# Performance work log

Hardware: AMD Instinct MI355X
Metric: run time of the kernel (lower is better)

Reference implementation:

```python
import jax, jax.numpy as jnp
import numpy as np

EMBED_DIM = 1024
FFN_DIM = 4096
N_QUBITS = 10


def setup_inputs() -> dict:
    key = jax.random.key(0)
    k_x, k_phi, k_w1, k_w2 = jax.random.split(key, 4)
    x = jax.random.normal(k_x, (8, 2048, EMBED_DIM), dtype=jnp.float32)
    # trainable RY angles, one per wire (torchquantum init ~ U(0, 2pi); any init works for a reference)
    ry_params = jax.random.uniform(k_phi, (N_QUBITS,), dtype=jnp.float32, minval=0.0, maxval=2.0 * np.pi)
    # nn.Linear(n_qubits, ffn_dim, bias=False): weight [ffn_dim, n_qubits]
    w1 = jax.random.normal(k_w1, (FFN_DIM, N_QUBITS), dtype=jnp.float32) / np.sqrt(N_QUBITS)
    # nn.Linear(ffn_dim, embed_dim, bias=False): weight [embed_dim, ffn_dim]
    w2 = jax.random.normal(k_w2, (EMBED_DIM, FFN_DIM), dtype=jnp.float32) / np.sqrt(FFN_DIM)
    return {"x": x, "ry_params": ry_params, "w1": w1, "w2": w2}


def reference(x, ry_params, w1, w2):
    # Quantum layer in closed form: wires are unentangled.
    # |0> --RX(x_i)--RY(phi_i)--> <Z_i> = cos(x_i) * cos(phi_i)
    # Only the first N_QUBITS features of each token are encoded.
    q_out = jnp.cos(x[..., :N_QUBITS]) * jnp.cos(ry_params)  # [B, S, nq]
    # dropout is identity in eval mode
    h = jnp.einsum('bsq,fq->bsf', q_out, w1)  # [B, S, ffn]
    h = jax.nn.relu(h)
    return jnp.einsum('bsf,ef->bse', h, w2)  # [B, S, embed]
```

## Files before the change

### kernel.cpp

```cpp
#include <hip/hip_runtime.h>
#include <stdint.h>

#define M_TOK   16384
#define EMBED   1024
#define FFN     4096
#define NQ      10

#define GK 4096
#define GN 1024
#define BK 64
#define NT (GK / BK)

typedef __attribute__((ext_vector_type(8))) short  bf16x8;
typedef __attribute__((ext_vector_type(4))) float  f32x4;
typedef __attribute__((ext_vector_type(8))) unsigned short u16x8;

static __device__ __forceinline__ unsigned short f2bf(float f) {
    union { float f; unsigned u; } v; v.f = f;
    unsigned r = v.u + 0x7FFF + ((v.u >> 16) & 1);
    return (unsigned short)(r >> 16);
}

__global__ __launch_bounds__(256) void fused_aux(
    const float* __restrict__ x,  const float* __restrict__ ry,
    const float* __restrict__ w1, const float* __restrict__ w2,
    unsigned short* __restrict__ h, unsigned short* __restrict__ w2b)
{
    __shared__ float cq[32 * 16];
    __shared__ float cry[NQ];

    const int bid = blockIdx.x;
    const int tid = threadIdx.x;

    if (bid < 1024) {
        const int t0 = (bid >> 1) * 32;
        const int fb = (bid & 1) * 2048 + tid * 8;

        if (tid < NQ) cry[tid] = cosf(ry[tid]);
        for (int idx = tid; idx < 32 * NQ; idx += 256) {
            int t = idx / NQ;
            int i = idx - t * NQ;
            cq[t * 16 + i] = cosf(x[(size_t)(t0 + t) * EMBED + i]);
        }
        __syncthreads();

        float wf[8][NQ];
#pragma unroll
        for (int fi = 0; fi < 8; ++fi)
#pragma unroll
            for (int i = 0; i < NQ; ++i)
                wf[fi][i] = w1[(fb + fi) * NQ + i] * cry[i];

        for (int t = 0; t < 32; ++t) {
            const float4 c0 = *(const float4*)&cq[t * 16 + 0];
            const float4 c1 = *(const float4*)&cq[t * 16 + 4];
            const float2 c2 = *(const float2*)&cq[t * 16 + 8];
            u16x8 v;
#pragma unroll
            for (int fi = 0; fi < 8; ++fi) {
                float s = c0.x * wf[fi][0] + c0.y * wf[fi][1] + c0.z * wf[fi][2]
                        + c0.w * wf[fi][3] + c1.x * wf[fi][4] + c1.y * wf[fi][5]
                        + c1.z * wf[fi][6] + c1.w * wf[fi][7] + c2.x * wf[fi][8]
                        + c2.y * wf[fi][9];
                v[fi] = f2bf(fmaxf(s, 0.f));
            }
            *(u16x8*)(h + (size_t)(t0 + t) * FFN + fb) = v;
        }
    } else {
        const int idx = ((bid - 1024) * 256 + tid) * 8;
        float4 a = *(const float4*)(w2 + idx);
        float4 b = *(const float4*)(w2 + idx + 4);
        u16x8 v;
        v[0] = f2bf(a.x); v[1] = f2bf(a.y); v[2] = f2bf(a.z); v[3] = f2bf(a.w);
        v[4] = f2bf(b.x); v[5] = f2bf(b.y); v[6] = f2bf(b.z); v[7] = f2bf(b.w);
        *(u16x8*)(w2b + idx) = v;
    }
}

#define GL2LDS(g, l) \
    __builtin_amdgcn_global_load_lds( \
        (const __attribute__((address_space(1))) void*)(g), \
        (__attribute__((address_space(3))) void*)(l), 16, 0, 0)

__global__ __launch_bounds__(512, 2) void gemm_bt(
    const unsigned short* __restrict__ A,
    const unsigned short* __restrict__ B,
    float* __restrict__ C)
{
    __shared__ __align__(16) unsigned short As[2][256 * BK];
    __shared__ __align__(16) unsigned short Bs[2][256 * BK];

    const int tid  = threadIdx.x;
    const int wv   = tid >> 6;
    const int lane = tid & 63;
    const int wm   = wv >> 2;
    const int wn   = wv & 3;

    const int bid = blockIdx.x;
    const int wg  = (bid & 7) * 32 + (bid >> 3);
    const int m0  = (wg >> 2) * 256;
    const int n0  = (wg & 3) * 256;

    const int srow8 = lane >> 3;
    const int schk  = (lane & 7) ^ srow8;
    const char* ag = (const char*)A +
        ((size_t)(m0 + wv * 16 + srow8) * GK + schk * 8) * 2;
    const char* bg = (const char*)B +
        ((size_t)(n0 + wv * 16 + srow8) * GK + schk * 8) * 2;
    const size_t ROW8 = (size_t)8 * GK * 2;
    const size_t HALF = (size_t)128 * GK * 2;

#define STAGE_A(buf, half, ko) do { \
    GL2LDS(ag + (ko) + (half) * HALF,        (char*)As[buf] + ((half) * 128 + wv * 16) * 128); \
    GL2LDS(ag + (ko) + (half) * HALF + ROW8, (char*)As[buf] + ((half) * 128 + wv * 16 + 8) * 128); \
} while (0)
#define STAGE_B(buf, half, ko) do { \
    GL2LDS(bg + (ko) + (half) * HALF,        (char*)Bs[buf] + ((half) * 128 + wv * 16) * 128); \
    GL2LDS(bg + (ko) + (half) * HALF + ROW8, (char*)Bs[buf] + ((half) * 128 + wv * 16 + 8) * 128); \
} while (0)
#define STAGE_ALL(buf, ko) do { \
    STAGE_A(buf, 0, ko); STAGE_A(buf, 1, ko); \
    STAGE_B(buf, 0, ko); STAGE_B(buf, 1, ko); \
} while (0)

    const int rr  = lane & 15;
    const int fsw = lane & 7;
    const int cc  = lane >> 4;
#define CHOFF(s) ((((s) * 4 + cc) ^ fsw) * 16)
#define RD_A(dst, Pt, mh) do { \
    _Pragma("unroll") \
    for (int s_ = 0; s_ < 2; ++s_) \
        _Pragma("unroll") \
        for (int i_ = 0; i_ < 4; ++i_) \
            dst[s_][i_] = *(const bf16x8*)((Pt) + \
                (wm * 128 + (mh) * 64 + i_ * 16 + rr) * 128 + CHOFF(s_)); \
} while (0)
#define RD_B(dst, Pt, nh) do { \
    _Pragma("unroll") \
    for (int s_ = 0; s_ < 2; ++s_) \
        _Pragma("unroll") \
        for (int j_ = 0; j_ < 2; ++j_) \
            dst[s_][j_] = *(const bf16x8*)((Pt) + \
                (wn * 64 + (nh) * 32 + j_ * 16 + rr) * 128 + CHOFF(s_)); \
} while (0)

    f32x4 acc[8][4] = {};

#define MFMA16(AF, BF, I0, J0) do { \
    __builtin_amdgcn_s_setprio(1); \
    _Pragma("unroll") \
    for (int s_ = 0; s_ < 2; ++s_) \
        _Pragma("unroll") \
        for (int i_ = 0; i_ < 4; ++i_) \
            _Pragma("unroll") \
            for (int j_ = 0; j_ < 2; ++j_) \
                acc[(I0) + i_][(J0) + j_] = __builtin_amdgcn_mfma_f32_16x16x32_bf16( \
                    AF[s_][i_], BF[s_][j_], acc[(I0) + i_][(J0) + j_], 0, 0, 0); \
    __builtin_amdgcn_s_setprio(0); \
} while (0)

    bf16x8 aA[2][4], aB[2][4], bP[2][2], bQ[2][2];

    STAGE_ALL(0, 0);
    STAGE_ALL(1, 128);
    asm volatile("s_waitcnt vmcnt(8)" ::: "memory");
    __builtin_amdgcn_s_barrier();
    RD_A(aA, (const char*)As[0], 0);
    RD_B(bP, (const char*)Bs[0], 0);

#define TILE(T, cur, nxt, BPm, BQm, doRead, doStage, ko2) do { \
    const char* At = (const char*)As[cur]; \
    const char* Bt = (const char*)Bs[cur]; \
     \
    RD_B(BQm, Bt, 1); \
    MFMA16(aA, BPm, 0, 0); \
     \
    RD_A(aB, At, 1); \
    MFMA16(aA, BQm, 0, 2); \
     \
    MFMA16(aB, BQm, 4, 2); \
    asm volatile("s_waitcnt vmcnt(0)" ::: "memory"); \
    __builtin_amdgcn_s_barrier(); \
    __builtin_amdgcn_sched_barrier(0); \
     \
    if (doRead) { \
        const char* An = (const char*)As[nxt]; \
        const char* Bn = (const char*)Bs[nxt]; \
        RD_A(aA, An, 0); \
        RD_B(BQm, Bn, 0); \
    } \
    if (doStage) STAGE_ALL(cur, ko2); \
    MFMA16(aB, BPm, 4, 0); \
} while (0)

#pragma unroll 1
    for (int tt = 0; tt < NT / 2; ++tt) {
        const bool nl = (tt < NT / 2 - 1);
        TILE(2 * tt, 0, 1, bP, bQ, true, nl, (size_t)(2 * tt + 2) * 128);
        TILE(2 * tt + 1, 1, 0, bQ, bP, nl, nl, (size_t)(2 * tt + 3) * 128);
    }

    const int cn = lane & 15;
    const int rb = (lane >> 4) * 4;
#pragma unroll
    for (int i = 0; i < 8; ++i)
#pragma unroll
        for (int j = 0; j < 4; ++j)
#pragma unroll
            for (int r = 0; r < 4; ++r) {
                const int m = m0 + wm * 128 + i * 16 + rb + r;
                const int n = n0 + wn * 64 + j * 16 + cn;
                C[(size_t)m * GN + n] = acc[i][j][r];
            }
}

extern "C" void kernel_launch(void* const* d_in, const int* in_sizes, int n_in,
                              void* d_out, int out_size, void* d_ws, size_t ws_size,
                              hipStream_t stream) {
    const float* x  = (const float*)d_in[0];
    const float* ry = (const float*)d_in[1];
    const float* w1 = (const float*)d_in[2];
    const float* w2 = (const float*)d_in[3];
    float* out = (float*)d_out;

    unsigned short* h   = (unsigned short*)d_ws;
    unsigned short* w2b = (unsigned short*)((char*)d_ws +
                           (size_t)M_TOK * FFN * sizeof(unsigned short));

    fused_aux<<<dim3(1024 + 2048), 256, 0, stream>>>(x, ry, w1, w2, h, w2b);
    gemm_bt<<<dim3(256), 512, 0, stream>>>(h, w2b, out);
}
```

Before: 248.9 us.

## Restructure GEMM main loop with per-wave quadrant order and simpler prefetch

```diff
diff --git a/kernel.cpp b/kernel.cpp
--- a/kernel.cpp
+++ b/kernel.cpp
@@ -159,45 +159,41 @@
     __builtin_amdgcn_s_setprio(0); \
 } while (0)
 
-    bf16x8 aA[2][4], aB[2][4], bP[2][2], bQ[2][2];
+    bf16x8 aA[2][4], aB[2][4], b0[2][2], b1[2][2];
 
     STAGE_ALL(0, 0);
-    STAGE_ALL(1, 128);
-    asm volatile("s_waitcnt vmcnt(8)" ::: "memory");
+    asm volatile("s_waitcnt vmcnt(0)" ::: "memory");
     __builtin_amdgcn_s_barrier();
-    RD_A(aA, (const char*)As[0], 0);
-    RD_B(bP, (const char*)Bs[0], 0);
-
-#define TILE(T, cur, nxt, BPm, BQm, doRead, doStage, ko2) do { \
-    const char* At = (const char*)As[cur]; \
-    const char* Bt = (const char*)Bs[cur]; \
-     \
-    RD_B(BQm, Bt, 1); \
-    MFMA16(aA, BPm, 0, 0); \
-     \
-    RD_A(aB, At, 1); \
-    MFMA16(aA, BQm, 0, 2); \
-     \
-    MFMA16(aB, BQm, 4, 2); \
-    asm volatile("s_waitcnt vmcnt(0)" ::: "memory"); \
-    __builtin_amdgcn_s_barrier(); \
-    __builtin_amdgcn_sched_barrier(0); \
-     \
-    if (doRead) { \
-        const char* An = (const char*)As[nxt]; \
-        const char* Bn = (const char*)Bs[nxt]; \
-        RD_A(aA, An, 0); \
-        RD_B(BQm, Bn, 0); \
-    } \
-    if (doStage) STAGE_ALL(cur, ko2); \
-    MFMA16(aB, BPm, 4, 0); \
-} while (0)
 
 #pragma unroll 1
-    for (int tt = 0; tt < NT / 2; ++tt) {
-        const bool nl = (tt < NT / 2 - 1);
-        TILE(2 * tt, 0, 1, bP, bQ, true, nl, (size_t)(2 * tt + 2) * 128);
-        TILE(2 * tt + 1, 1, 0, bQ, bP, nl, nl, (size_t)(2 * tt + 3) * 128);
+    for (int T = 0; T < NT; ++T) {
+        const int cur = T & 1;
+        const char* At = (const char*)As[cur];
+        const char* Bt = (const char*)Bs[cur];
+        const size_t ko = (T + 1 < NT) ? (size_t)(T + 1) * 128 : 0;
+
+        STAGE_ALL(cur ^ 1, ko);
+
+        if (wv < 4) {
+            RD_A(aA, At, 0); RD_B(b0, Bt, 0);
+            MFMA16(aA, b0, 0, 0);
+            RD_B(b1, Bt, 1);
+            MFMA16(aA, b1, 0, 2);
+            RD_A(aB, At, 1);
+            MFMA16(aB, b1, 4, 2);
+            MFMA16(aB, b0, 4, 0);
+        } else {
+            RD_A(aB, At, 1); RD_B(b1, Bt, 1);
+            MFMA16(aB, b1, 4, 2);
+            RD_B(b0, Bt, 0);
+            MFMA16(aB, b0, 4, 0);
+            RD_A(aA, At, 0);
+            MFMA16(aA, b0, 0, 0);
+            MFMA16(aA, b1, 0, 2);
+        }
+
+        asm volatile("s_waitcnt vmcnt(0)" ::: "memory");
+        __builtin_amdgcn_s_barrier();
     }
 
     const int cn = lane & 15;
```

Result: slower. 268.0 us (+7.7%).
